# Kernel optimization log

Hardware: AMD Instinct MI355X
Metric: run time of the kernel (lower is better)

The kernel has to match this reference:

```python
import jax, jax.numpy as jnp
import numpy as np

N_SRC = 50000
N_DST = 50000
E = 800000
IN_DIM = 128
OUT_DIM = 64
HEADS = 4
NEG_SLOPE = 0.2  # PyG GATConv default negative_slope
EPS = 1e-16      # PyG softmax denominator epsilon


def setup_inputs() -> dict:
    key = jax.random.key(0)
    ks = jax.random.split(key, 8)
    x_src = jax.random.normal(ks[0], (N_SRC, IN_DIM), dtype=jnp.float32)
    x_dst = jax.random.normal(ks[1], (N_DST, IN_DIM), dtype=jnp.float32)
    src = jax.random.randint(ks[2], (E,), 0, N_SRC, dtype=jnp.int32)
    dst = jax.random.randint(ks[3], (E,), 0, N_DST, dtype=jnp.int32)
    edge_index = jnp.stack([src, dst], axis=0)
    W_src = jax.random.normal(ks[4], (IN_DIM, HEADS * OUT_DIM), dtype=jnp.float32) / np.sqrt(IN_DIM)
    W_dst = jax.random.normal(ks[5], (IN_DIM, HEADS * OUT_DIM), dtype=jnp.float32) / np.sqrt(IN_DIM)
    att_src = jax.random.normal(ks[6], (HEADS, OUT_DIM), dtype=jnp.float32) / np.sqrt(OUT_DIM)
    att_dst = jax.random.normal(ks[7], (HEADS, OUT_DIM), dtype=jnp.float32) / np.sqrt(OUT_DIM)
    bias = jnp.zeros((OUT_DIM,), dtype=jnp.float32)
    return {"x_src": x_src, "x_dst": x_dst, "edge_index": edge_index,
            "W_src": W_src, "W_dst": W_dst, "att_src": att_src,
            "att_dst": att_dst, "bias": bias}


def reference(x_src, x_dst, edge_index, W_src, W_dst, att_src, att_dst, bias):
    # Linear projections -> [N, H, C]
    hs = (x_src @ W_src).reshape(N_SRC, HEADS, OUT_DIM)
    hd = (x_dst @ W_dst).reshape(N_DST, HEADS, OUT_DIM)
    # Per-node attention logits -> [N, H]
    a_s = jnp.einsum('nhc,hc->nh', hs, att_src)
    a_d = jnp.einsum('nhc,hc->nh', hd, att_dst)

    src, dst = edge_index[0], edge_index[1]
    # Per-edge logits [E, H]
    alpha = jax.nn.leaky_relu(a_s[src] + a_d[dst], negative_slope=NEG_SLOPE)
    # Segment softmax over edges sharing the same dst node
    amax = jax.ops.segment_max(alpha, dst, num_segments=N_DST)
    alpha = jnp.exp(alpha - amax[dst])
    denom = jax.ops.segment_sum(alpha, dst, num_segments=N_DST)
    alpha = alpha / (denom[dst] + EPS)
    # (dropout=0 / eval mode: no attention dropout)
    # Message + scatter-add aggregation: out[i] = sum_e alpha_e * hs[src_e]
    msg = hs[src] * alpha[:, :, None]                 # [E, H, C]
    out = jax.ops.segment_sum(msg, dst, num_segments=N_DST)  # [N_dst, H, C]
    # concat=False -> mean over heads, then bias
    return out.mean(axis=1) + bias
```

## Files before the change

kernel.cpp:

```cpp
#include <hip/hip_runtime.h>
#include <hip/hip_bf16.h>

#define N_SRC 50000
#define N_DST 50000
#define NEDGE 800000
#define IND   128
#define HEADS 4
#define CDIM  64
#define HC    256
#define NB_SCAN 49
#define NB_ALPHA 12500
#define NB_HIST  3125

typedef _Float16 half8  __attribute__((ext_vector_type(8)));
typedef _Float16 half2t __attribute__((ext_vector_type(2)));
typedef float    f32x4  __attribute__((ext_vector_type(4)));

static __device__ __forceinline__ unsigned int pack2h(float a, float b) {
    union { half2t h; unsigned int u; } v;
    v.h[0] = (_Float16)a; v.h[1] = (_Float16)b;
    return v.u;
}
static __device__ __forceinline__ half2t bits2h(unsigned int u) {
    union { unsigned int u; half2t h; } v; v.u = u; return v.h;
}

__global__ void prep_kernel(const float* __restrict__ Wdst,
                            const float* __restrict__ att_d,
                            float* __restrict__ WdA,
                            const float* __restrict__ Wsrc,
                            _Float16* __restrict__ WhT, int* __restrict__ deg) {
    int b = blockIdx.x, tid = threadIdx.x;
    if (b < 196) {
        int i = b * 256 + tid;
        if (i < N_DST) deg[i] = 0;
    } else if (b < 198) {
        int id = (b - 196) * 256 + tid;
        int k = id >> 2, h = id & 3;
        float acc = 0.f;
        for (int c = 0; c < CDIM; ++c)
            acc += Wdst[k * HC + h * CDIM + c] * att_d[h * CDIM + c];
        WdA[id] = acc;
    } else {
        int idx = (b - 198) * 256 + tid;
        int n = idx >> 7, k = idx & 127;
        WhT[idx] = (_Float16)Wsrc[k * HC + n];
    }
}

__global__ __launch_bounds__(256) void gemm_mfma_kernel(
        const float* __restrict__ x, const _Float16* __restrict__ WhT,
        const float* __restrict__ att_s,
        unsigned short* __restrict__ hsTh, float* __restrict__ a_s) {
    int tid = threadIdx.x;
    int w = tid >> 6, lane = tid & 63;
    int ll = lane & 15, q = lane >> 4;
    int rbase = blockIdx.x * 64 + w * 16;

    int arow = rbase + ll;
    if (arow >= N_SRC) arow = N_SRC - 1;
    const float* xr = x + (size_t)arow * IND + q * 8;
    half8 afrag[4];
    #pragma unroll
    for (int kf = 0; kf < 4; ++kf) {
        float4 u0 = *(const float4*)(xr + kf * 32);
        float4 u1 = *(const float4*)(xr + kf * 32 + 4);
        half8 a;
        a[0] = (_Float16)u0.x; a[1] = (_Float16)u0.y;
        a[2] = (_Float16)u0.z; a[3] = (_Float16)u0.w;
        a[4] = (_Float16)u1.x; a[5] = (_Float16)u1.y;
        a[6] = (_Float16)u1.z; a[7] = (_Float16)u1.w;
        afrag[kf] = a;
    }

    f32x4 acc[16];
    #pragma unroll
    for (int t = 0; t < 16; ++t) acc[t] = (f32x4){0.f, 0.f, 0.f, 0.f};

    #pragma unroll
    for (int t = 0; t < 16; ++t) {
        const _Float16* bp = WhT + (size_t)(t * 16 + ll) * IND + q * 8;
        half8 b0 = *(const half8*)(bp + 0);
        half8 b1 = *(const half8*)(bp + 32);
        half8 b2 = *(const half8*)(bp + 64);
        half8 b3 = *(const half8*)(bp + 96);
        f32x4 c = acc[t];
        c = __builtin_amdgcn_mfma_f32_16x16x32_f16(afrag[0], b0, c, 0, 0, 0);
        c = __builtin_amdgcn_mfma_f32_16x16x32_f16(afrag[1], b1, c, 0, 0, 0);
        c = __builtin_amdgcn_mfma_f32_16x16x32_f16(afrag[2], b2, c, 0, 0, 0);
        c = __builtin_amdgcn_mfma_f32_16x16x32_f16(afrag[3], b3, c, 0, 0, 0);
        acc[t] = c;
    }

    #pragma unroll
    for (int tg = 0; tg < 4; ++tg) {
        #pragma unroll
        for (int r = 0; r < 4; ++r) {
            int n = rbase + q * 4 + r;
            if (n < N_SRC) {
                uint2 v;
                v.x = pack2h(acc[tg     ][r], acc[tg + 4 ][r]);
                v.y = pack2h(acc[tg + 8 ][r], acc[tg + 12][r]);
                *(uint2*)(hsTh + (size_t)n * HC + (tg * 16 + ll) * 4) = v;
            }
        }
    }

    float attv[16];
    #pragma unroll
    for (int t = 0; t < 16; ++t) attv[t] = att_s[t * 16 + ll];
    #pragma unroll
    for (int r = 0; r < 4; ++r) {
        float4 p;
        p.x = acc[0][r]*attv[0]  + acc[1][r]*attv[1]  + acc[2][r]*attv[2]  + acc[3][r]*attv[3];
        p.y = acc[4][r]*attv[4]  + acc[5][r]*attv[5]  + acc[6][r]*attv[6]  + acc[7][r]*attv[7];
        p.z = acc[8][r]*attv[8]  + acc[9][r]*attv[9]  + acc[10][r]*attv[10]+ acc[11][r]*attv[11];
        p.w = acc[12][r]*attv[12]+ acc[13][r]*attv[13]+ acc[14][r]*attv[14]+ acc[15][r]*attv[15];
        #pragma unroll
        for (int off = 1; off < 16; off <<= 1) {
            p.x += __shfl_xor(p.x, off, 64);
            p.y += __shfl_xor(p.y, off, 64);
            p.z += __shfl_xor(p.z, off, 64);
            p.w += __shfl_xor(p.w, off, 64);
        }
        int n = rbase + q * 4 + r;
        if (ll == 0 && n < N_SRC) *(float4*)(a_s + (size_t)n * 4) = p;
    }
}

__global__ __launch_bounds__(256) void mid_kernel(
        const float* __restrict__ x_dst, const float* __restrict__ WdA,
        float* __restrict__ a_d,
        const int* __restrict__ dst, int* __restrict__ deg, int* __restrict__ rank) {
    int b = blockIdx.x, tid = threadIdx.x;
    if (b < NB_ALPHA) {
        int n    = (b * 256 + tid) >> 6;
        int lane = tid & 63;
        const float* xp = x_dst + (size_t)n * IND;
        const float4* wa = (const float4*)WdA;
        float x0 = xp[lane], x1 = xp[lane + 64];
        float4 wa0 = wa[lane], wa1 = wa[lane + 64];
        float p0 = x0 * wa0.x + x1 * wa1.x;
        float p1 = x0 * wa0.y + x1 * wa1.y;
        float p2 = x0 * wa0.z + x1 * wa1.z;
        float p3 = x0 * wa0.w + x1 * wa1.w;
        for (int off = 32; off >= 1; off >>= 1) {
            p0 += __shfl_xor(p0, off, 64);
            p1 += __shfl_xor(p1, off, 64);
            p2 += __shfl_xor(p2, off, 64);
            p3 += __shfl_xor(p3, off, 64);
        }
        if (lane == 0) {
            a_d[n * 4 + 0] = p0; a_d[n * 4 + 1] = p1;
            a_d[n * 4 + 2] = p2; a_d[n * 4 + 3] = p3;
        }
    } else {
        int e = (b - NB_ALPHA) * 256 + tid;
        if (e < NEDGE) rank[e] = atomicAdd(&deg[dst[e]], 1);
    }
}

__global__ __launch_bounds__(256) void scan_part_kernel(const int* __restrict__ deg,
                                                        int* __restrict__ partial) {
    __shared__ int wsum[4];
    int tid = threadIdx.x, lane = tid & 63, wid = tid >> 6;
    int i0 = blockIdx.x * 1024 + tid * 4;
    int s = 0;
    #pragma unroll
    for (int j = 0; j < 4; ++j) if (i0 + j < N_DST) s += deg[i0 + j];
    for (int off = 32; off >= 1; off >>= 1) s += __shfl_xor(s, off, 64);
    if (lane == 0) wsum[wid] = s;
    __syncthreads();
    if (tid == 0) partial[blockIdx.x] = wsum[0] + wsum[1] + wsum[2] + wsum[3];
}

__global__ __launch_bounds__(256) void scan_write_kernel(const int* __restrict__ deg,
                                                         const int* __restrict__ partial,
                                                         int* __restrict__ row_ptr) {
    __shared__ int wsum[4];
    __shared__ int block_off;
    int tid = threadIdx.x, lane = tid & 63, wid = tid >> 6;
    if (tid < 64) {
        int v = (lane < NB_SCAN) ? partial[lane] : 0;
        int xx = v;
        for (int off = 1; off < 64; off <<= 1) {
            int u = __shfl_up(xx, off, 64);
            if (lane >= off) xx += u;
        }
        if (lane == blockIdx.x) block_off = xx - v;
    }
    int i0 = blockIdx.x * 1024 + tid * 4;
    int v0 = (i0 + 0 < N_DST) ? deg[i0 + 0] : 0;
    int v1 = (i0 + 1 < N_DST) ? deg[i0 + 1] : 0;
    int v2 = (i0 + 2 < N_DST) ? deg[i0 + 2] : 0;
    int v3 = (i0 + 3 < N_DST) ? deg[i0 + 3] : 0;
    int t1 = v0, t2 = t1 + v1, t3 = t2 + v2, t4 = t3 + v3;
    int x = t4;
    for (int off = 1; off < 64; off <<= 1) {
        int u = __shfl_up(x, off, 64);
        if (lane >= off) x += u;
    }
    int wave_excl = x - t4;
    if (lane == 63) wsum[wid] = x;
    __syncthreads();
    int woff = 0;
    for (int k = 0; k < wid; ++k) woff += wsum[k];
    int tb = block_off + woff + wave_excl;
    if (i0 + 0 < N_DST) row_ptr[i0 + 0] = tb;
    if (i0 + 1 < N_DST) row_ptr[i0 + 1] = tb + t1;
    if (i0 + 2 < N_DST) row_ptr[i0 + 2] = tb + t2;
    if (i0 + 3 < N_DST) row_ptr[i0 + 3] = tb + t3;
    if (blockIdx.x == 0 && tid == 0) row_ptr[N_DST] = NEDGE;
}

__global__ void scatter_kernel(const int* __restrict__ src, const int* __restrict__ dst,
                               const int* __restrict__ row_ptr,
                               const int* __restrict__ rank, int* __restrict__ col) {
    int e = blockIdx.x * 256 + threadIdx.x;
    if (e >= NEDGE) return;
    int d = dst[e];
    col[row_ptr[d] + rank[e]] = src[e];
}

__global__ __launch_bounds__(256) void aggregate_kernel(
        const int* __restrict__ row_ptr, const int* __restrict__ col,
        const float4* __restrict__ as4, const float4* __restrict__ ad4,
        const unsigned short* __restrict__ hsTh,
        const float* __restrict__ bias, float* __restrict__ out) {
    __shared__ uint4 s_pk[4][64];
    int tid = threadIdx.x;
    int wv = tid >> 6, lane = tid & 63;
    int i = (blockIdx.x * 256 + tid) >> 6;
    if (i >= N_DST) return;
    int beg = row_ptr[i], end = row_ptr[i + 1];
    float bv = bias[lane];
    if (beg == end) { out[i * CDIM + lane] = bv; return; }
    float4 ad = ad4[i];

    float s0 = 0.f, s1 = 0.f, s2 = 0.f, s3 = 0.f;
    for (int cb = beg; cb < end; cb += 64) {
        int e = cb + lane;
        bool valid = e < end;
        int sn = valid ? col[e] : 0;
        float4 av = as4[sn];
        float lx = av.x + ad.x; lx = lx > 0.f ? lx : 0.2f * lx;
        float ly = av.y + ad.y; ly = ly > 0.f ? ly : 0.2f * ly;
        float lz = av.z + ad.z; lz = lz > 0.f ? lz : 0.2f * lz;
        float lw = av.w + ad.w; lw = lw > 0.f ? lw : 0.2f * lw;
        s0 += valid ? __expf(lx) : 0.f;
        s1 += valid ? __expf(ly) : 0.f;
        s2 += valid ? __expf(lz) : 0.f;
        s3 += valid ? __expf(lw) : 0.f;
    }
    for (int off = 32; off >= 1; off >>= 1) {
        s0 += __shfl_xor(s0, off, 64);
        s1 += __shfl_xor(s1, off, 64);
        s2 += __shfl_xor(s2, off, 64);
        s3 += __shfl_xor(s3, off, 64);
    }
    float i0 = 0.25f / (s0 + 1e-16f);
    float i1 = 0.25f / (s1 + 1e-16f);
    float i2 = 0.25f / (s2 + 1e-16f);
    float i3 = 0.25f / (s3 + 1e-16f);

    const unsigned short* hb = hsTh + (lane << 2);
    float acc = 0.f;
    for (int cb = beg; cb < end; cb += 64) {
        int e = cb + lane;
        bool valid = e < end;
        int sn = valid ? col[e] : 0;
        float4 av = as4[sn];
        float lx = av.x + ad.x; lx = lx > 0.f ? lx : 0.2f * lx;
        float ly = av.y + ad.y; ly = ly > 0.f ? ly : 0.2f * ly;
        float lz = av.z + ad.z; lz = lz > 0.f ? lz : 0.2f * lz;
        float lw = av.w + ad.w; lw = lw > 0.f ? lw : 0.2f * lw;
        float w0 = valid ? __expf(lx) * i0 : 0.f;
        float w1 = valid ? __expf(ly) * i1 : 0.f;
        float w2 = valid ? __expf(lz) * i2 : 0.f;
        float w3 = valid ? __expf(lw) * i3 : 0.f;
        uint4 pk;
        pk.x = (unsigned int)(sn * HC);
        pk.y = pack2h(w0, w1);
        pk.z = pack2h(w2, w3);
        pk.w = 0;
        s_pk[wv][lane] = pk;
        __asm__ volatile("s_waitcnt lgkmcnt(0)" ::: "memory");

        int cnt = end - cb; if (cnt > 64) cnt = 64;
        int j = 0;
        for (; j + 4 <= cnt; j += 4) {
            uint4 p0 = s_pk[wv][j];
            uint4 p1 = s_pk[wv][j + 1];
            uint4 p2 = s_pk[wv][j + 2];
            uint4 p3 = s_pk[wv][j + 3];
            uint2 h0 = *(const uint2*)(hb + p0.x);
            uint2 h1 = *(const uint2*)(hb + p1.x);
            uint2 h2 = *(const uint2*)(hb + p2.x);
            uint2 h3 = *(const uint2*)(hb + p3.x);
            acc = __builtin_amdgcn_fdot2(bits2h(h0.x), bits2h(p0.y), acc, false);
            acc = __builtin_amdgcn_fdot2(bits2h(h0.y), bits2h(p0.z), acc, false);
            acc = __builtin_amdgcn_fdot2(bits2h(h1.x), bits2h(p1.y), acc, false);
            acc = __builtin_amdgcn_fdot2(bits2h(h1.y), bits2h(p1.z), acc, false);
            acc = __builtin_amdgcn_fdot2(bits2h(h2.x), bits2h(p2.y), acc, false);
            acc = __builtin_amdgcn_fdot2(bits2h(h2.y), bits2h(p2.z), acc, false);
            acc = __builtin_amdgcn_fdot2(bits2h(h3.x), bits2h(p3.y), acc, false);
            acc = __builtin_amdgcn_fdot2(bits2h(h3.y), bits2h(p3.z), acc, false);
        }
        for (; j < cnt; ++j) {
            uint4 p0 = s_pk[wv][j];
            uint2 h0 = *(const uint2*)(hb + p0.x);
            acc = __builtin_amdgcn_fdot2(bits2h(h0.x), bits2h(p0.y), acc, false);
            acc = __builtin_amdgcn_fdot2(bits2h(h0.y), bits2h(p0.z), acc, false);
        }
    }
    out[i * CDIM + lane] = acc + bv;
}

extern "C" void kernel_launch(void* const* d_in, const int* in_sizes, int n_in,
                              void* d_out, int out_size, void* d_ws, size_t ws_size,
                              hipStream_t stream) {
    const float* x_src   = (const float*)d_in[0];
    const float* x_dst   = (const float*)d_in[1];
    const int*   ei      = (const int*)d_in[2];
    const float* W_src   = (const float*)d_in[3];
    const float* W_dst   = (const float*)d_in[4];
    const float* att_src = (const float*)d_in[5];
    const float* att_dst = (const float*)d_in[6];
    const float* bias    = (const float*)d_in[7];
    float* out = (float*)d_out;

    char* ws = (char*)d_ws;
    unsigned short* hsTh = (unsigned short*)ws; ws += (size_t)N_SRC * HC * 2;
    int*    col     = (int*)ws;    ws += (size_t)NEDGE * 4;
    int*    rank    = (int*)ws;    ws += (size_t)NEDGE * 4;
    float*  a_s     = (float*)ws;  ws += (size_t)N_SRC * 4 * 4;
    float*  a_d     = (float*)ws;  ws += (size_t)N_DST * 4 * 4;
    float*  WdA     = (float*)ws;  ws += 2048;
    _Float16* WhT   = (_Float16*)ws; ws += IND * HC * 2;
    int*    row_ptr = (int*)ws;    ws += 50004 * 4;
    int*    deg     = (int*)ws;    ws += N_DST * 4;
    int*    partial = (int*)ws;    ws += 64 * 4;

    prep_kernel<<<326, 256, 0, stream>>>(W_dst, att_dst, WdA, W_src, WhT, deg);
    gemm_mfma_kernel<<<(N_SRC + 63) / 64, 256, 0, stream>>>(x_src, WhT, att_src, hsTh, a_s);
    mid_kernel<<<NB_ALPHA + NB_HIST, 256, 0, stream>>>(x_dst, WdA, a_d, ei + NEDGE, deg, rank);
    scan_part_kernel<<<NB_SCAN, 256, 0, stream>>>(deg, partial);
    scan_write_kernel<<<NB_SCAN, 256, 0, stream>>>(deg, partial, row_ptr);
    scatter_kernel<<<NEDGE / 256, 256, 0, stream>>>(ei, ei + NEDGE, row_ptr, rank, col);
    aggregate_kernel<<<(N_DST + 3) / 4, 256, 0, stream>>>(row_ptr, col,
                                                          (const float4*)a_s, (const float4*)a_d,
                                                          hsTh, bias, out);
}
```

Baseline: 260.6 us.

## Merge CSR build and aggregation into one cooperative persistent kernel

Replaces five launches (dst-logit plus histogram, two scan passes, scatter, aggregate) with a single cooperative kernel of 1024 blocks that loops grid-stride over work and uses grid.sync between phases. This is meant to remove per-launch overhead and inter-kernel gaps. The risks are grid-barrier cost, low utilisation during the scan phases where only 49 blocks do work, and the persistent wave-per-node loop possibly balancing load worse than one wave per node. It also splits the LDS packing into separate offset and weight arrays.

```diff
diff --git a/kernel.cpp b/kernel.cpp
--- a/kernel.cpp
+++ b/kernel.cpp
@@ -1,5 +1,8 @@
 #include <hip/hip_runtime.h>
 #include <hip/hip_bf16.h>
+#include <hip/hip_cooperative_groups.h>
+
+namespace cg = cooperative_groups;
 
 #define N_SRC 50000
 #define N_DST 50000
@@ -9,8 +12,9 @@
 #define CDIM  64
 #define HC    256
 #define NB_SCAN 49
-#define NB_ALPHA 12500
-#define NB_HIST  3125
+#define NBLK   1024
+#define NWAVES (NBLK * 4)
+#define NTHR   (NBLK * 256)
 
 typedef _Float16 half8  __attribute__((ext_vector_type(8)));
 typedef _Float16 half2t __attribute__((ext_vector_type(2)));
@@ -128,192 +132,191 @@
     }
 }
 
-__global__ __launch_bounds__(256) void mid_kernel(
+__global__ __launch_bounds__(256, 4) void coop_kernel(
         const float* __restrict__ x_dst, const float* __restrict__ WdA,
         float* __restrict__ a_d,
-        const int* __restrict__ dst, int* __restrict__ deg, int* __restrict__ rank) {
-    int b = blockIdx.x, tid = threadIdx.x;
-    if (b < NB_ALPHA) {
-        int n    = (b * 256 + tid) >> 6;
-        int lane = tid & 63;
-        const float* xp = x_dst + (size_t)n * IND;
+        const int* __restrict__ src, const int* __restrict__ dst,
+        int* __restrict__ deg, int* __restrict__ rank,
+        int* __restrict__ partial, int* __restrict__ row_ptr,
+        int* __restrict__ col,
+        const float4* __restrict__ as4, const unsigned short* __restrict__ hsTh,
+        const float* __restrict__ bias, float* __restrict__ out) {
+    cg::grid_group grid = cg::this_grid();
+    __shared__ int          s_off[4][64];
+    __shared__ uint2        s_w[4][64];
+    __shared__ int          wsum[4];
+    __shared__ int          block_off;
+
+    int tid  = threadIdx.x;
+    int wv   = tid >> 6, lane = tid & 63;
+    int gt   = blockIdx.x * 256 + tid;
+    int gwave = gt >> 6;
+
+    {
         const float4* wa = (const float4*)WdA;
-        float x0 = xp[lane], x1 = xp[lane + 64];
         float4 wa0 = wa[lane], wa1 = wa[lane + 64];
-        float p0 = x0 * wa0.x + x1 * wa1.x;
-        float p1 = x0 * wa0.y + x1 * wa1.y;
-        float p2 = x0 * wa0.z + x1 * wa1.z;
-        float p3 = x0 * wa0.w + x1 * wa1.w;
-        for (int off = 32; off >= 1; off >>= 1) {
-            p0 += __shfl_xor(p0, off, 64);
-            p1 += __shfl_xor(p1, off, 64);
-            p2 += __shfl_xor(p2, off, 64);
-            p3 += __shfl_xor(p3, off, 64);
-        }
-        if (lane == 0) {
-            a_d[n * 4 + 0] = p0; a_d[n * 4 + 1] = p1;
-            a_d[n * 4 + 2] = p2; a_d[n * 4 + 3] = p3;
-        }
-    } else {
-        int e = (b - NB_ALPHA) * 256 + tid;
-        if (e < NEDGE) rank[e] = atomicAdd(&deg[dst[e]], 1);
-    }
-}
-
-__global__ __launch_bounds__(256) void scan_part_kernel(const int* __restrict__ deg,
-                                                        int* __restrict__ partial) {
-    __shared__ int wsum[4];
-    int tid = threadIdx.x, lane = tid & 63, wid = tid >> 6;
-    int i0 = blockIdx.x * 1024 + tid * 4;
-    int s = 0;
-    #pragma unroll
-    for (int j = 0; j < 4; ++j) if (i0 + j < N_DST) s += deg[i0 + j];
-    for (int off = 32; off >= 1; off >>= 1) s += __shfl_xor(s, off, 64);
-    if (lane == 0) wsum[wid] = s;
-    __syncthreads();
-    if (tid == 0) partial[blockIdx.x] = wsum[0] + wsum[1] + wsum[2] + wsum[3];
-}
-
-__global__ __launch_bounds__(256) void scan_write_kernel(const int* __restrict__ deg,
-                                                         const int* __restrict__ partial,
-                                                         int* __restrict__ row_ptr) {
-    __shared__ int wsum[4];
-    __shared__ int block_off;
-    int tid = threadIdx.x, lane = tid & 63, wid = tid >> 6;
-    if (tid < 64) {
-        int v = (lane < NB_SCAN) ? partial[lane] : 0;
-        int xx = v;
+        for (int n = gwave; n < N_DST; n += NWAVES) {
+            const float* xp = x_dst + (size_t)n * IND;
+            float x0 = xp[lane], x1 = xp[lane + 64];
+            float p0 = x0 * wa0.x + x1 * wa1.x;
+            float p1 = x0 * wa0.y + x1 * wa1.y;
+            float p2 = x0 * wa0.z + x1 * wa1.z;
+            float p3 = x0 * wa0.w + x1 * wa1.w;
+            for (int off = 32; off >= 1; off >>= 1) {
+                p0 += __shfl_xor(p0, off, 64);
+                p1 += __shfl_xor(p1, off, 64);
+                p2 += __shfl_xor(p2, off, 64);
+                p3 += __shfl_xor(p3, off, 64);
+            }
+            if (lane == 0) {
+                a_d[n * 4 + 0] = p0; a_d[n * 4 + 1] = p1;
+                a_d[n * 4 + 2] = p2; a_d[n * 4 + 3] = p3;
+            }
+        }
+    }
+    for (int e = gt; e < NEDGE; e += NTHR)
+        rank[e] = atomicAdd(&deg[dst[e]], 1);
+
+    grid.sync();
+
+    if (blockIdx.x < NB_SCAN) {
+        int i0 = blockIdx.x * 1024 + tid * 4;
+        int s = 0;
+        #pragma unroll
+        for (int j = 0; j < 4; ++j) if (i0 + j < N_DST) s += deg[i0 + j];
+        for (int off = 32; off >= 1; off >>= 1) s += __shfl_xor(s, off, 64);
+        if (lane == 0) wsum[wv] = s;
+        __syncthreads();
+        if (tid == 0) partial[blockIdx.x] = wsum[0] + wsum[1] + wsum[2] + wsum[3];
+    }
+
+    grid.sync();
+
+    if (blockIdx.x < NB_SCAN) {
+        if (tid < 64) {
+            int v = (lane < NB_SCAN) ? partial[lane] : 0;
+            int xx = v;
+            for (int off = 1; off < 64; off <<= 1) {
+                int u = __shfl_up(xx, off, 64);
+                if (lane >= off) xx += u;
+            }
+            if (lane == blockIdx.x) block_off = xx - v;
+        }
+        int i0 = blockIdx.x * 1024 + tid * 4;
+        int v0 = (i0 + 0 < N_DST) ? deg[i0 + 0] : 0;
+        int v1 = (i0 + 1 < N_DST) ? deg[i0 + 1] : 0;
+        int v2 = (i0 + 2 < N_DST) ? deg[i0 + 2] : 0;
+        int v3 = (i0 + 3 < N_DST) ? deg[i0 + 3] : 0;
+        int t1 = v0, t2 = t1 + v1, t3 = t2 + v2, t4 = t3 + v3;
+        int x = t4;
         for (int off = 1; off < 64; off <<= 1) {
-            int u = __shfl_up(xx, off, 64);
-            if (lane >= off) xx += u;
-        }
-        if (lane == blockIdx.x) block_off = xx - v;
-    }
-    int i0 = blockIdx.x * 1024 + tid * 4;
-    int v0 = (i0 + 0 < N_DST) ? deg[i0 + 0] : 0;
-    int v1 = (i0 + 1 < N_DST) ? deg[i0 + 1] : 0;
-    int v2 = (i0 + 2 < N_DST) ? deg[i0 + 2] : 0;
-    int v3 = (i0 + 3 < N_DST) ? deg[i0 + 3] : 0;
-    int t1 = v0, t2 = t1 + v1, t3 = t2 + v2, t4 = t3 + v3;
-    int x = t4;
-    for (int off = 1; off < 64; off <<= 1) {
-        int u = __shfl_up(x, off, 64);
-        if (lane >= off) x += u;
-    }
-    int wave_excl = x - t4;
-    if (lane == 63) wsum[wid] = x;
-    __syncthreads();
-    int woff = 0;
-    for (int k = 0; k < wid; ++k) woff += wsum[k];
-    int tb = block_off + woff + wave_excl;
-    if (i0 + 0 < N_DST) row_ptr[i0 + 0] = tb;
-    if (i0 + 1 < N_DST) row_ptr[i0 + 1] = tb + t1;
-    if (i0 + 2 < N_DST) row_ptr[i0 + 2] = tb + t2;
-    if (i0 + 3 < N_DST) row_ptr[i0 + 3] = tb + t3;
-    if (blockIdx.x == 0 && tid == 0) row_ptr[N_DST] = NEDGE;
-}
-
-__global__ void scatter_kernel(const int* __restrict__ src, const int* __restrict__ dst,
-                               const int* __restrict__ row_ptr,
-                               const int* __restrict__ rank, int* __restrict__ col) {
-    int e = blockIdx.x * 256 + threadIdx.x;
-    if (e >= NEDGE) return;
-    int d = dst[e];
-    col[row_ptr[d] + rank[e]] = src[e];
-}
-
-__global__ __launch_bounds__(256) void aggregate_kernel(
-        const int* __restrict__ row_ptr, const int* __restrict__ col,
-        const float4* __restrict__ as4, const float4* __restrict__ ad4,
-        const unsigned short* __restrict__ hsTh,
-        const float* __restrict__ bias, float* __restrict__ out) {
-    __shared__ uint4 s_pk[4][64];
-    int tid = threadIdx.x;
-    int wv = tid >> 6, lane = tid & 63;
-    int i = (blockIdx.x * 256 + tid) >> 6;
-    if (i >= N_DST) return;
-    int beg = row_ptr[i], end = row_ptr[i + 1];
-    float bv = bias[lane];
-    if (beg == end) { out[i * CDIM + lane] = bv; return; }
-    float4 ad = ad4[i];
-
-    float s0 = 0.f, s1 = 0.f, s2 = 0.f, s3 = 0.f;
-    for (int cb = beg; cb < end; cb += 64) {
-        int e = cb + lane;
-        bool valid = e < end;
-        int sn = valid ? col[e] : 0;
-        float4 av = as4[sn];
-        float lx = av.x + ad.x; lx = lx > 0.f ? lx : 0.2f * lx;
-        float ly = av.y + ad.y; ly = ly > 0.f ? ly : 0.2f * ly;
-        float lz = av.z + ad.z; lz = lz > 0.f ? lz : 0.2f * lz;
-        float lw = av.w + ad.w; lw = lw > 0.f ? lw : 0.2f * lw;
-        s0 += valid ? __expf(lx) : 0.f;
-        s1 += valid ? __expf(ly) : 0.f;
-        s2 += valid ? __expf(lz) : 0.f;
-        s3 += valid ? __expf(lw) : 0.f;
-    }
-    for (int off = 32; off >= 1; off >>= 1) {
-        s0 += __shfl_xor(s0, off, 64);
-        s1 += __shfl_xor(s1, off, 64);
-        s2 += __shfl_xor(s2, off, 64);
-        s3 += __shfl_xor(s3, off, 64);
-    }
-    float i0 = 0.25f / (s0 + 1e-16f);
-    float i1 = 0.25f / (s1 + 1e-16f);
-    float i2 = 0.25f / (s2 + 1e-16f);
-    float i3 = 0.25f / (s3 + 1e-16f);
-
-    const unsigned short* hb = hsTh + (lane << 2);
-    float acc = 0.f;
-    for (int cb = beg; cb < end; cb += 64) {
-        int e = cb + lane;
-        bool valid = e < end;
-        int sn = valid ? col[e] : 0;
-        float4 av = as4[sn];
-        float lx = av.x + ad.x; lx = lx > 0.f ? lx : 0.2f * lx;
-        float ly = av.y + ad.y; ly = ly > 0.f ? ly : 0.2f * ly;
-        float lz = av.z + ad.z; lz = lz > 0.f ? lz : 0.2f * lz;
-        float lw = av.w + ad.w; lw = lw > 0.f ? lw : 0.2f * lw;
-        float w0 = valid ? __expf(lx) * i0 : 0.f;
-        float w1 = valid ? __expf(ly) * i1 : 0.f;
-        float w2 = valid ? __expf(lz) * i2 : 0.f;
-        float w3 = valid ? __expf(lw) * i3 : 0.f;
-        uint4 pk;
-        pk.x = (unsigned int)(sn * HC);
-        pk.y = pack2h(w0, w1);
-        pk.z = pack2h(w2, w3);
-        pk.w = 0;
-        s_pk[wv][lane] = pk;
-        __asm__ volatile("s_waitcnt lgkmcnt(0)" ::: "memory");
-
-        int cnt = end - cb; if (cnt > 64) cnt = 64;
-        int j = 0;
-        for (; j + 4 <= cnt; j += 4) {
-            uint4 p0 = s_pk[wv][j];
-            uint4 p1 = s_pk[wv][j + 1];
-            uint4 p2 = s_pk[wv][j + 2];
-            uint4 p3 = s_pk[wv][j + 3];
-            uint2 h0 = *(const uint2*)(hb + p0.x);
-            uint2 h1 = *(const uint2*)(hb + p1.x);
-            uint2 h2 = *(const uint2*)(hb + p2.x);
-            uint2 h3 = *(const uint2*)(hb + p3.x);
-            acc = __builtin_amdgcn_fdot2(bits2h(h0.x), bits2h(p0.y), acc, false);
-            acc = __builtin_amdgcn_fdot2(bits2h(h0.y), bits2h(p0.z), acc, false);
-            acc = __builtin_amdgcn_fdot2(bits2h(h1.x), bits2h(p1.y), acc, false);
-            acc = __builtin_amdgcn_fdot2(bits2h(h1.y), bits2h(p1.z), acc, false);
-            acc = __builtin_amdgcn_fdot2(bits2h(h2.x), bits2h(p2.y), acc, false);
-            acc = __builtin_amdgcn_fdot2(bits2h(h2.y), bits2h(p2.z), acc, false);
-            acc = __builtin_amdgcn_fdot2(bits2h(h3.x), bits2h(p3.y), acc, false);
-            acc = __builtin_amdgcn_fdot2(bits2h(h3.y), bits2h(p3.z), acc, false);
-        }
-        for (; j < cnt; ++j) {
-            uint4 p0 = s_pk[wv][j];
-            uint2 h0 = *(const uint2*)(hb + p0.x);
-            acc = __builtin_amdgcn_fdot2(bits2h(h0.x), bits2h(p0.y), acc, false);
-            acc = __builtin_amdgcn_fdot2(bits2h(h0.y), bits2h(p0.z), acc, false);
-        }
-    }
-    out[i * CDIM + lane] = acc + bv;
+            int u = __shfl_up(x, off, 64);
+            if (lane >= off) x += u;
+        }
+        int wave_excl = x - t4;
+        if (lane == 63) wsum[wv] = x;
+        __syncthreads();
+        int woff = 0;
+        for (int k = 0; k < wv; ++k) woff += wsum[k];
+        int tb = block_off + woff + wave_excl;
+        if (i0 + 0 < N_DST) row_ptr[i0 + 0] = tb;
+        if (i0 + 1 < N_DST) row_ptr[i0 + 1] = tb + t1;
+        if (i0 + 2 < N_DST) row_ptr[i0 + 2] = tb + t2;
+        if (i0 + 3 < N_DST) row_ptr[i0 + 3] = tb + t3;
+        if (blockIdx.x == 0 && tid == 0) row_ptr[N_DST] = NEDGE;
+    }
+
+    grid.sync();
+
+    for (int e = gt; e < NEDGE; e += NTHR)
+        col[row_ptr[dst[e]] + rank[e]] = src[e];
+
+    grid.sync();
+
+    {
+        const float4* ad4 = (const float4*)a_d;
+        float bv = bias[lane];
+        const unsigned short* hb = hsTh + (lane << 2);
+        for (int i = gwave; i < N_DST; i += NWAVES) {
+            int beg = row_ptr[i], end = row_ptr[i + 1];
+            if (beg == end) { out[i * CDIM + lane] = bv; continue; }
+            float4 ad = ad4[i];
+
+            float s0 = 0.f, s1 = 0.f, s2 = 0.f, s3 = 0.f;
+            for (int cb = beg; cb < end; cb += 64) {
+                int e = cb + lane;
+                bool valid = e < end;
+                int sn = valid ? col[e] : 0;
+                float4 av = as4[sn];
+                float lx = av.x + ad.x; lx = lx > 0.f ? lx : 0.2f * lx;
+                float ly = av.y + ad.y; ly = ly > 0.f ? ly : 0.2f * ly;
+                float lz = av.z + ad.z; lz = lz > 0.f ? lz : 0.2f * lz;
+                float lw = av.w + ad.w; lw = lw > 0.f ? lw : 0.2f * lw;
+                s0 += valid ? __expf(lx) : 0.f;
+                s1 += valid ? __expf(ly) : 0.f;
+                s2 += valid ? __expf(lz) : 0.f;
+                s3 += valid ? __expf(lw) : 0.f;
+            }
+            for (int off = 32; off >= 1; off >>= 1) {
+                s0 += __shfl_xor(s0, off, 64);
+                s1 += __shfl_xor(s1, off, 64);
+                s2 += __shfl_xor(s2, off, 64);
+                s3 += __shfl_xor(s3, off, 64);
+            }
+            float i0 = 0.25f / (s0 + 1e-16f);
+            float i1 = 0.25f / (s1 + 1e-16f);
+            float i2 = 0.25f / (s2 + 1e-16f);
+            float i3 = 0.25f / (s3 + 1e-16f);
+
+            float acc = 0.f;
+            for (int cb = beg; cb < end; cb += 64) {
+                int e = cb + lane;
+                bool valid = e < end;
+                int sn = valid ? col[e] : 0;
+                float4 av = as4[sn];
+                float lx = av.x + ad.x; lx = lx > 0.f ? lx : 0.2f * lx;
+                float ly = av.y + ad.y; ly = ly > 0.f ? ly : 0.2f * ly;
+                float lz = av.z + ad.z; lz = lz > 0.f ? lz : 0.2f * lz;
+                float lw = av.w + ad.w; lw = lw > 0.f ? lw : 0.2f * lw;
+                float w0 = valid ? __expf(lx) * i0 : 0.f;
+                float w1 = valid ? __expf(ly) * i1 : 0.f;
+                float w2 = valid ? __expf(lz) * i2 : 0.f;
+                float w3 = valid ? __expf(lw) * i3 : 0.f;
+                s_off[wv][lane] = sn * HC;
+                uint2 wp; wp.x = pack2h(w0, w1); wp.y = pack2h(w2, w3);
+                s_w[wv][lane] = wp;
+                __asm__ volatile("s_waitcnt lgkmcnt(0)" ::: "memory");
+
+                int cnt = end - cb; if (cnt > 64) cnt = 64;
+                int j = 0;
+                for (; j + 4 <= cnt; j += 4) {
+                    int  o0 = s_off[wv][j];     uint2 p0 = s_w[wv][j];
+                    int  o1 = s_off[wv][j + 1]; uint2 p1 = s_w[wv][j + 1];
+                    int  o2 = s_off[wv][j + 2]; uint2 p2 = s_w[wv][j + 2];
+                    int  o3 = s_off[wv][j + 3]; uint2 p3 = s_w[wv][j + 3];
+                    uint2 h0 = *(const uint2*)(hb + o0);
+                    uint2 h1 = *(const uint2*)(hb + o1);
+                    uint2 h2 = *(const uint2*)(hb + o2);
+                    uint2 h3 = *(const uint2*)(hb + o3);
+                    acc = __builtin_amdgcn_fdot2(bits2h(h0.x), bits2h(p0.x), acc, false);
+                    acc = __builtin_amdgcn_fdot2(bits2h(h0.y), bits2h(p0.y), acc, false);
+                    acc = __builtin_amdgcn_fdot2(bits2h(h1.x), bits2h(p1.x), acc, false);
+                    acc = __builtin_amdgcn_fdot2(bits2h(h1.y), bits2h(p1.y), acc, false);
+                    acc = __builtin_amdgcn_fdot2(bits2h(h2.x), bits2h(p2.x), acc, false);
+                    acc = __builtin_amdgcn_fdot2(bits2h(h2.y), bits2h(p2.y), acc, false);
+                    acc = __builtin_amdgcn_fdot2(bits2h(h3.x), bits2h(p3.x), acc, false);
+                    acc = __builtin_amdgcn_fdot2(bits2h(h3.y), bits2h(p3.y), acc, false);
+                }
+                for (; j < cnt; ++j) {
+                    int o0 = s_off[wv][j]; uint2 p0 = s_w[wv][j];
+                    uint2 h0 = *(const uint2*)(hb + o0);
+                    acc = __builtin_amdgcn_fdot2(bits2h(h0.x), bits2h(p0.x), acc, false);
+                    acc = __builtin_amdgcn_fdot2(bits2h(h0.y), bits2h(p0.y), acc, false);
+                }
+            }
+            out[i * CDIM + lane] = acc + bv;
+        }
+    }
 }
 
 extern "C" void kernel_launch(void* const* d_in, const int* in_sizes, int n_in,
@@ -343,11 +346,16 @@
 
     prep_kernel<<<326, 256, 0, stream>>>(W_dst, att_dst, WdA, W_src, WhT, deg);
     gemm_mfma_kernel<<<(N_SRC + 63) / 64, 256, 0, stream>>>(x_src, WhT, att_src, hsTh, a_s);
-    mid_kernel<<<NB_ALPHA + NB_HIST, 256, 0, stream>>>(x_dst, WdA, a_d, ei + NEDGE, deg, rank);
-    scan_part_kernel<<<NB_SCAN, 256, 0, stream>>>(deg, partial);
-    scan_write_kernel<<<NB_SCAN, 256, 0, stream>>>(deg, partial, row_ptr);
-    scatter_kernel<<<NEDGE / 256, 256, 0, stream>>>(ei, ei + NEDGE, row_ptr, rank, col);
-    aggregate_kernel<<<(N_DST + 3) / 4, 256, 0, stream>>>(row_ptr, col,
-                                                          (const float4*)a_s, (const float4*)a_d,
-                                                          hsTh, bias, out);
-}
+
+    const int* srcp = ei;
+    const int* dstp = ei + NEDGE;
+    const float4* as4 = (const float4*)a_s;
+    void* kargs[] = {
+        (void*)&x_dst, (void*)&WdA, (void*)&a_d,
+        (void*)&srcp, (void*)&dstp,
+        (void*)&deg, (void*)&rank, (void*)&partial, (void*)&row_ptr,
+        (void*)&col, (void*)&as4, (void*)&hsTh, (void*)&bias, (void*)&out
+    };
+    hipLaunchCooperativeKernel((void*)coop_kernel, dim3(NBLK), dim3(256),
+                               kargs, 0, stream);
+}
```

New measurement: 728.8 us. 2.8x slower.
